# Performance work log

Hardware: AMD Instinct MI355X
Metric: run time of the kernel (lower is better)

Reference implementation:

```python
import jax, jax.numpy as jnp
import numpy as np

B, N, D, H = 2, 4096, 256, 8
HD = D // H
NEG_SLOPE = 0.01
LN_EPS = 1e-5


def setup_inputs() -> dict:
    key = jax.random.key(0)
    ks = jax.random.split(key, 6)
    s = 1.0 / np.sqrt(D)
    return {
        "h": jax.random.normal(ks[0], (B, N, D), dtype=jnp.float32),
        "W_l": jax.random.normal(ks[1], (D, D), dtype=jnp.float32) * s,
        "W_r": jax.random.normal(ks[2], (D, D), dtype=jnp.float32) * s,
        "a_l": jax.random.normal(ks[3], (HD,), dtype=jnp.float32) * s,
        "a_r": jax.random.normal(ks[4], (HD,), dtype=jnp.float32) * s,
        "W_final": jax.random.normal(ks[5], (D, D), dtype=jnp.float32) * s,
        "ln_g": jnp.ones((D,), dtype=jnp.float32),
        "ln_b": jnp.zeros((D,), dtype=jnp.float32),
    }


def _leaky(x):
    return jnp.where(x >= 0, x, NEG_SLOPE * x)


def reference(h, W_l, W_r, a_l, a_r, W_final, ln_g, ln_b):
    b, n, d = h.shape
    # projections -> [b, H, n, HD]
    fl = (h @ W_l).reshape(b, n, H, HD).transpose(0, 2, 1, 3)
    fr = (h @ W_r).reshape(b, n, H, HD).transpose(0, 2, 1, 3)
    # additive GAT-style scores: [b, H, n] each, broadcast to [b, H, n, n]
    sl = jnp.einsum("bhnd,d->bhn", _leaky(fl), a_l)
    sr = jnp.einsum("bhnd,d->bhn", _leaky(fr), a_r)
    score = sl[..., :, None] + sr[..., None, :]  # [b, H, n, n]
    attn = jnp.mean(score, axis=1)  # pre-softmax mean over heads: [b, n, n]
    p = jax.nn.softmax(score, axis=-1)  # dropout is identity (eval / p=0)
    context = jnp.einsum("bhij,bhjd->bhid", p, fr)  # [b, H, n, HD]
    h_sa = context.transpose(0, 2, 1, 3).reshape(b, n, d)
    fh = h_sa @ W_final
    x = h + fh
    mu = jnp.mean(x, axis=-1, keepdims=True)
    var = jnp.mean(jnp.square(x - mu), axis=-1, keepdims=True)
    h_out = (x - mu) * jax.lax.rsqrt(var + LN_EPS) * ln_g + ln_b
    return (h_out, attn)
```

## Files before the change

kernel.cpp:

```cpp
#include <hip/hip_runtime.h>
#include <hip/hip_bf16.h>

#define BATCH 2
#define SEQ   4096
#define DIM   256
#define HEADS 8
#define HDIM  32
#define M_ROWS (BATCH * SEQ)
#define FPSCALE 4294967296.0

typedef short bf16x8 __attribute__((ext_vector_type(8)));
typedef unsigned short u16x8 __attribute__((ext_vector_type(8)));
typedef float f32x4 __attribute__((ext_vector_type(4)));

static __device__ inline unsigned short f2bf(float x) {
  union { float f; unsigned u; } v; v.f = x;
  unsigned r = v.u + 0x7FFF + ((v.u >> 16) & 1);
  return (unsigned short)(r >> 16);
}

__global__ __launch_bounds__(256) void k_prep(const float* __restrict__ Wl,
                                              const float* __restrict__ Wr,
                                              unsigned short* __restrict__ Wt,
                                              unsigned long long* __restrict__ yctx,
                                              unsigned long long* __restrict__ wacc) {
  if (blockIdx.y == 0) {
    const int idx = blockIdx.x * 256 + threadIdx.x;
    if (idx < BATCH * DIM) yctx[idx] = 0ull;
    if (idx < BATCH * HEADS) wacc[idx] = 0ull;
  }
  __shared__ float tile[32][33];
  const int k0 = blockIdx.x * 32;
  const int n0 = blockIdx.y * 32;
  const int t = threadIdx.x;
  const float* W = (n0 < 256) ? Wl : Wr;
  const int nb = n0 & 255;
  {
    const int r = t >> 3;
    const int c = (t & 7) * 4;
    const float4 v = *(const float4*)(&W[(size_t)(k0 + r) * DIM + nb + c]);
    tile[r][c + 0] = v.x; tile[r][c + 1] = v.y;
    tile[r][c + 2] = v.z; tile[r][c + 3] = v.w;
  }
  __syncthreads();
  {
    const int nl = t >> 3;
    const int kl = (t & 7) * 4;
    ushort4 o;
    o.x = f2bf(tile[kl + 0][nl]); o.y = f2bf(tile[kl + 1][nl]);
    o.z = f2bf(tile[kl + 2][nl]); o.w = f2bf(tile[kl + 3][nl]);
    *(ushort4*)(&Wt[(size_t)(n0 + nl) * DIM + k0 + kl]) = o;
  }
}

__global__ __launch_bounds__(512) void k_gemm_fused(
    const float* __restrict__ A, const unsigned short* __restrict__ Wt,
    const float* __restrict__ a_l, const float* __restrict__ a_r,
    float* __restrict__ msl, float* __restrict__ msr,
    unsigned long long* __restrict__ yctx,
    unsigned long long* __restrict__ wacc) {
  __shared__ unsigned short As[64 * 32];
  __shared__ unsigned short Bs[256 * 32];
  __shared__ float red[64][8];

  const int bid = blockIdx.x;
  const int isR = bid & 1;
  const int bm  = bid >> 1;
  const int m0 = bm * 64;
  const int n0 = isR * 256;

  const int t = threadIdx.x;
  const int lane = t & 63;
  const int wid = t >> 6;

  f32x4 acc[4][2];
  #pragma unroll
  for (int i = 0; i < 4; ++i)
    #pragma unroll
    for (int j = 0; j < 2; ++j) acc[i][j] = (f32x4){0.f, 0.f, 0.f, 0.f};

  for (int k0 = 0; k0 < DIM; k0 += 32) {
    if (t < 256) {
      const int row = t >> 2;
      const int kc = t & 3;
      const int slot = kc ^ ((row >> 1) & 3);
      const float4 a0 = *(const float4*)(&A[(size_t)(m0 + row) * DIM + k0 + kc * 8]);
      const float4 a1 = *(const float4*)(&A[(size_t)(m0 + row) * DIM + k0 + kc * 8 + 4]);
      u16x8 pa;
      pa[0] = f2bf(a0.x); pa[1] = f2bf(a0.y); pa[2] = f2bf(a0.z); pa[3] = f2bf(a0.w);
      pa[4] = f2bf(a1.x); pa[5] = f2bf(a1.y); pa[6] = f2bf(a1.z); pa[7] = f2bf(a1.w);
      *(u16x8*)((char*)As + row * 64 + slot * 16) = pa;
    }
    #pragma unroll
    for (int p = 0; p < 2; ++p) {
      const int task = t + p * 512;
      const int row = task >> 2;
      const int kc = task & 3;
      const int slot = kc ^ ((row >> 1) & 3);
      const u16x8 pb = *(const u16x8*)(&Wt[(size_t)(n0 + row) * DIM + k0 + kc * 8]);
      *(u16x8*)((char*)Bs + row * 64 + slot * 16) = pb;
    }
    __syncthreads();

    bf16x8 af[4], bfr[2];
    #pragma unroll
    for (int mr = 0; mr < 4; ++mr) {
      const int ra = mr * 16 + (lane & 15);
      const int sl = (lane >> 4) ^ ((ra >> 1) & 3);
      af[mr] = *(const bf16x8*)((const char*)As + ra * 64 + sl * 16);
    }
    #pragma unroll
    for (int nr = 0; nr < 2; ++nr) {
      const int cb = wid * 32 + nr * 16 + (lane & 15);
      const int sl = (lane >> 4) ^ ((cb >> 1) & 3);
      bfr[nr] = *(const bf16x8*)((const char*)Bs + cb * 64 + sl * 16);
    }
    #pragma unroll
    for (int mr = 0; mr < 4; ++mr)
      #pragma unroll
      for (int nr = 0; nr < 2; ++nr)
        acc[mr][nr] = __builtin_amdgcn_mfma_f32_16x16x32_bf16(af[mr], bfr[nr], acc[mr][nr], 0, 0, 0);
    __syncthreads();
  }

  const float* av = isR ? a_r : a_l;
  const int b = m0 >> 12;

  float e[4][4];
  #pragma unroll
  for (int mr = 0; mr < 4; ++mr) {
    #pragma unroll
    for (int r = 0; r < 4; ++r) {
      float p = 0.f;
      #pragma unroll
      for (int nr = 0; nr < 2; ++nr) {
        float x = acc[mr][nr][r];
        x = x >= 0.f ? x : 0.01f * x;
        p = fmaf(x, av[nr * 16 + (lane & 15)], p);
      }
      #pragma unroll
      for (int o = 1; o < 16; o <<= 1) p += __shfl_xor(p, o, 16);
      if ((lane & 15) == 0) {
        const int rl = mr * 16 + (lane >> 4) * 4 + r;
        red[rl][wid] = p;
      }
      e[mr][r] = __expf(p) ;
    }
  }

  if (isR) {
    float se = 0.f;
    #pragma unroll
    for (int mr = 0; mr < 4; ++mr)
      #pragma unroll
      for (int r = 0; r < 4; ++r) se += e[mr][r];
    se += __shfl_xor(se, 16, 64);
    se += __shfl_xor(se, 32, 64);
    if (lane == 0)
      atomicAdd(&wacc[b * HEADS + wid],
                (unsigned long long)__double2ll_rn((double)se * FPSCALE));
    #pragma unroll
    for (int nr = 0; nr < 2; ++nr) {
      float y = 0.f;
      #pragma unroll
      for (int mr = 0; mr < 4; ++mr)
        #pragma unroll
        for (int r = 0; r < 4; ++r)
          y = fmaf(e[mr][r], acc[mr][nr][r], y);
      y += __shfl_xor(y, 16, 64);
      y += __shfl_xor(y, 32, 64);
      if (lane < 16)
        atomicAdd(&yctx[(size_t)b * DIM + wid * 32 + nr * 16 + lane],
                  (unsigned long long)__double2ll_rn((double)y * FPSCALE));
    }
  }
  __syncthreads();
  if (t < 64) {
    float s = 0.f;
    #pragma unroll
    for (int h2 = 0; h2 < 8; ++h2) s += red[t][h2];
    (isR ? msr : msl)[m0 + t] = s * 0.125f;
  }
}

__global__ __launch_bounds__(256) void k_fh(const unsigned long long* __restrict__ yctx,
                                            const unsigned long long* __restrict__ wacc,
                                            const float* __restrict__ Wf,
                                            float* __restrict__ fh2) {
  const int b = blockIdx.x;
  const int t = threadIdx.x;
  __shared__ float c_s[DIM];
  c_s[t] = (float)((double)(long long)yctx[(size_t)b * DIM + t] /
                   (double)(long long)wacc[b * HEADS + (t >> 5)]);
  __syncthreads();
  float a2 = 0.f;
  #pragma unroll 8
  for (int k = 0; k < DIM; ++k)
    a2 = fmaf(c_s[k], Wf[(size_t)k * DIM + t], a2);
  fh2[b * DIM + t] = a2;
}

__global__ __launch_bounds__(256) void k_ln_attn(const float* __restrict__ h,
                                                 const float* __restrict__ fh2,
                                                 const float* __restrict__ g,
                                                 const float* __restrict__ bb,
                                                 const float* __restrict__ msl,
                                                 const float* __restrict__ msr,
                                                 float* __restrict__ out,
                                                 float* __restrict__ attn) {
  const int row0 = blockIdx.x * 2;
  const int b = row0 >> 12;
  const int t = threadIdx.x;

  const float fh = fh2[b * DIM + t];
  const float x0 = h[(size_t)row0 * DIM + t] + fh;
  const float x1 = h[(size_t)(row0 + 1) * DIM + t] + fh;
  float s10 = x0, s20 = x0 * x0, s11 = x1, s21 = x1 * x1;
  #pragma unroll
  for (int o = 32; o > 0; o >>= 1) {
    s10 += __shfl_xor(s10, o, 64);
    s20 += __shfl_xor(s20, o, 64);
    s11 += __shfl_xor(s11, o, 64);
    s21 += __shfl_xor(s21, o, 64);
  }
  __shared__ float r1[2][4], r2[2][4];
  if ((t & 63) == 0) {
    r1[0][t >> 6] = s10; r2[0][t >> 6] = s20;
    r1[1][t >> 6] = s11; r2[1][t >> 6] = s21;
  }
  __syncthreads();
  const float gs = g[t], bs = bb[t];
  {
    const float s1 = r1[0][0] + r1[0][1] + r1[0][2] + r1[0][3];
    const float s2 = r2[0][0] + r2[0][1] + r2[0][2] + r2[0][3];
    const float mu = s1 * (1.f / 256.f);
    const float var = s2 * (1.f / 256.f) - mu * mu;
    const float rs = rsqrtf(var + 1e-5f);
    out[(size_t)row0 * DIM + t] = (x0 - mu) * rs * gs + bs;
  }
  {
    const float s1 = r1[1][0] + r1[1][1] + r1[1][2] + r1[1][3];
    const float s2 = r2[1][0] + r2[1][1] + r2[1][2] + r2[1][3];
    const float mu = s1 * (1.f / 256.f);
    const float var = s2 * (1.f / 256.f) - mu * mu;
    const float rs = rsqrtf(var + 1e-5f);
    out[(size_t)(row0 + 1) * DIM + t] = (x1 - mu) * rs * gs + bs;
  }

  const float v0 = msl[row0];
  const float v1 = msl[row0 + 1];
  const f32x4* mr4 = (const f32x4*)(msr + ((size_t)b << 12));
  f32x4* dst0 = (f32x4*)(attn + ((size_t)row0 << 12));
  f32x4* dst1 = (f32x4*)(attn + ((size_t)(row0 + 1) << 12));
  #pragma unroll
  for (int q = 0; q < 4; ++q) {
    const f32x4 m4 = mr4[q * 256 + t];
    __builtin_nontemporal_store(m4 + v0, &dst0[q * 256 + t]);
    __builtin_nontemporal_store(m4 + v1, &dst1[q * 256 + t]);
  }
}

extern "C" void kernel_launch(void* const* d_in, const int* in_sizes, int n_in,
                              void* d_out, int out_size, void* d_ws, size_t ws_size,
                              hipStream_t stream) {
  const float* h  = (const float*)d_in[0];
  const float* Wl = (const float*)d_in[1];
  const float* Wr = (const float*)d_in[2];
  const float* al = (const float*)d_in[3];
  const float* ar = (const float*)d_in[4];
  const float* Wf = (const float*)d_in[5];
  const float* g  = (const float*)d_in[6];
  const float* bb = (const float*)d_in[7];
  float* out = (float*)d_out;

  unsigned long long* yctx = (unsigned long long*)d_ws;
  unsigned long long* wacc = yctx + BATCH * DIM;
  float* msl = (float*)(wacc + BATCH * HEADS);
  float* msr = msl + M_ROWS;
  float* fh2 = msr + M_ROWS;
  unsigned short* Wt = (unsigned short*)(fh2 + BATCH * DIM);

  k_prep<<<dim3(8, 16), 256, 0, stream>>>(Wl, Wr, Wt, yctx, wacc);
  k_gemm_fused<<<256, 512, 0, stream>>>(h, Wt, al, ar, msl, msr, yctx, wacc);
  k_fh<<<BATCH, 256, 0, stream>>>(yctx, wacc, Wf, fh2);
  k_ln_attn<<<M_ROWS / 2, 256, 0, stream>>>(h, fh2, g, bb, msl, msr,
                                            out, out + (size_t)M_ROWS * DIM);
}
```

Before: 57.05 us.

## Overlap tiny fh GEMV with attn broadcast writes in one kernel

Moves the 128 MB attn-matrix broadcast write out of the LayerNorm kernel and into the same launch as the small per-batch fh GEMV. Two blocks compute fh while the rest write attn rows. Each attn block now writes 4 rows and reuses one msr load held in registers. The serial k_fh launch, which occupied only two blocks, is hidden behind the bandwidth-bound store. The LayerNorm kernel becomes lightweight, and the launch count stays at four.

Result: slower. 59.68 us (+4.6%).

```diff
diff --git a/kernel.cpp b/kernel.cpp
--- a/kernel.cpp
+++ b/kernel.cpp
@@ -8,6 +8,8 @@
 #define HDIM  32
 #define M_ROWS (BATCH * SEQ)
 #define FPSCALE 4294967296.0
+#define ATTNROWS 4
+#define ATTNBLKS (M_ROWS / ATTNROWS)
 
 typedef short bf16x8 __attribute__((ext_vector_type(8)));
 typedef unsigned short u16x8 __attribute__((ext_vector_type(8)));
@@ -144,7 +146,7 @@
         const int rl = mr * 16 + (lane >> 4) * 4 + r;
         red[rl][wid] = p;
       }
-      e[mr][r] = __expf(p) ;
+      e[mr][r] = __expf(p);
     }
   }
 
@@ -183,31 +185,50 @@
   }
 }
 
-__global__ __launch_bounds__(256) void k_fh(const unsigned long long* __restrict__ yctx,
-                                            const unsigned long long* __restrict__ wacc,
-                                            const float* __restrict__ Wf,
-                                            float* __restrict__ fh2) {
-  const int b = blockIdx.x;
-  const int t = threadIdx.x;
-  __shared__ float c_s[DIM];
-  c_s[t] = (float)((double)(long long)yctx[(size_t)b * DIM + t] /
-                   (double)(long long)wacc[b * HEADS + (t >> 5)]);
-  __syncthreads();
-  float a2 = 0.f;
-  #pragma unroll 8
-  for (int k = 0; k < DIM; ++k)
-    a2 = fmaf(c_s[k], Wf[(size_t)k * DIM + t], a2);
-  fh2[b * DIM + t] = a2;
-}
-
-__global__ __launch_bounds__(256) void k_ln_attn(const float* __restrict__ h,
-                                                 const float* __restrict__ fh2,
-                                                 const float* __restrict__ g,
-                                                 const float* __restrict__ bb,
-                                                 const float* __restrict__ msl,
-                                                 const float* __restrict__ msr,
-                                                 float* __restrict__ out,
-                                                 float* __restrict__ attn) {
+__global__ __launch_bounds__(256) void k_attn_fh(
+    const float* __restrict__ msl, const float* __restrict__ msr,
+    const unsigned long long* __restrict__ yctx,
+    const unsigned long long* __restrict__ wacc,
+    const float* __restrict__ Wf,
+    float* __restrict__ fh2, float* __restrict__ attn) {
+  const int blk = blockIdx.x;
+  const int t = threadIdx.x;
+
+  if (blk < BATCH) {
+    const int b = blk;
+    __shared__ float c_s[DIM];
+    c_s[t] = (float)((double)(long long)yctx[(size_t)b * DIM + t] /
+                     (double)(long long)wacc[b * HEADS + (t >> 5)]);
+    __syncthreads();
+    float a2 = 0.f;
+    #pragma unroll 8
+    for (int k = 0; k < DIM; ++k)
+      a2 = fmaf(c_s[k], Wf[(size_t)k * DIM + t], a2);
+    fh2[b * DIM + t] = a2;
+    return;
+  }
+
+  const int row0 = (blk - BATCH) * ATTNROWS;
+  const int b = row0 >> 12;
+  f32x4 m[4];
+  const f32x4* mr4 = (const f32x4*)(msr + ((size_t)b << 12));
+  #pragma unroll
+  for (int q = 0; q < 4; ++q) m[q] = mr4[q * 256 + t];
+  #pragma unroll
+  for (int rr = 0; rr < ATTNROWS; ++rr) {
+    const float v = msl[row0 + rr];
+    f32x4* dst = (f32x4*)(attn + ((size_t)(row0 + rr) << 12));
+    #pragma unroll
+    for (int q = 0; q < 4; ++q)
+      __builtin_nontemporal_store(m[q] + v, &dst[q * 256 + t]);
+  }
+}
+
+__global__ __launch_bounds__(256) void k_ln(const float* __restrict__ h,
+                                            const float* __restrict__ fh2,
+                                            const float* __restrict__ g,
+                                            const float* __restrict__ bb,
+                                            float* __restrict__ out) {
   const int row0 = blockIdx.x * 2;
   const int b = row0 >> 12;
   const int t = threadIdx.x;
@@ -245,18 +266,6 @@
     const float var = s2 * (1.f / 256.f) - mu * mu;
     const float rs = rsqrtf(var + 1e-5f);
     out[(size_t)(row0 + 1) * DIM + t] = (x1 - mu) * rs * gs + bs;
-  }
-
-  const float v0 = msl[row0];
-  const float v1 = msl[row0 + 1];
-  const f32x4* mr4 = (const f32x4*)(msr + ((size_t)b << 12));
-  f32x4* dst0 = (f32x4*)(attn + ((size_t)row0 << 12));
-  f32x4* dst1 = (f32x4*)(attn + ((size_t)(row0 + 1) << 12));
-  #pragma unroll
-  for (int q = 0; q < 4; ++q) {
-    const f32x4 m4 = mr4[q * 256 + t];
-    __builtin_nontemporal_store(m4 + v0, &dst0[q * 256 + t]);
-    __builtin_nontemporal_store(m4 + v1, &dst1[q * 256 + t]);
   }
 }
 
@@ -282,7 +291,7 @@
 
   k_prep<<<dim3(8, 16), 256, 0, stream>>>(Wl, Wr, Wt, yctx, wacc);
   k_gemm_fused<<<256, 512, 0, stream>>>(h, Wt, al, ar, msl, msr, yctx, wacc);
-  k_fh<<<BATCH, 256, 0, stream>>>(yctx, wacc, Wf, fh2);
-  k_ln_attn<<<M_ROWS / 2, 256, 0, stream>>>(h, fh2, g, bb, msl, msr,
-                                            out, out + (size_t)M_ROWS * DIM);
-}
+  k_attn_fh<<<BATCH + ATTNBLKS, 256, 0, stream>>>(msl, msr, yctx, wacc, Wf,
+                                                  fh2, out + (size_t)M_ROWS * DIM);
+  k_ln<<<M_ROWS / 2, 256, 0, stream>>>(h, fh2, g, bb, out);
+}
```
